# Kernel tuning notes

Measured on AMD Instinct MI355X. Metric: run time of the kernel, lower is better.

The kernel has to match this reference:

```python
import jax, jax.numpy as jnp
import numpy as np

WORD_DIM = 200
ASPECT_DIM = 32
NUM_NEG = 2
AVG_RATING = 3.8
LR_RATING = 1.0
LR_ABAE = 1.0


def setup_inputs() -> dict:
    key = jax.random.key(0)
    ks = jax.random.split(key, 20)
    R, L, D, A, B, NNZ = 20000, 30, WORD_DIM, ASPECT_DIM, 4096, 65536
    e_w = jax.random.normal(ks[0], (R, L, D), jnp.float32)
    y_s = jax.random.normal(ks[1], (R, D), jnp.float32)
    z_n = jax.random.normal(ks[2], (R * NUM_NEG, D), jnp.float32)
    label = jax.random.uniform(ks[3], (B,), jnp.float32, 1.0, 5.0)
    u_idx = jnp.stack([jax.random.randint(ks[4], (NNZ,), 0, B),
                       jax.random.randint(ks[5], (NNZ,), 0, R)]).astype(jnp.int64)
    i_idx = jnp.stack([jax.random.randint(ks[6], (NNZ,), 0, B),
                       jax.random.randint(ks[7], (NNZ,), 0, R)]).astype(jnp.int64)
    u_val = jax.random.uniform(ks[8], (NNZ,), jnp.float32)
    i_val = jax.random.uniform(ks[9], (NNZ,), jnp.float32)
    s = 0.05
    M_w = jax.random.normal(ks[10], (D, D), jnp.float32) * s
    M_b = jnp.zeros((D,), jnp.float32)
    W_w = jax.random.normal(ks[11], (A, D), jnp.float32) * s
    W_b = jnp.zeros((A,), jnp.float32)
    T_w = jax.random.normal(ks[12], (D, A), jnp.float32) * s
    T_b = jnp.zeros((D,), jnp.float32)
    fc_w = jax.random.uniform(ks[13], (1, A), jnp.float32, -0.05, 0.05)
    fc_b = jnp.zeros((1,), jnp.float32)
    fm_V = jax.random.uniform(ks[14], (A, 10), jnp.float32, -0.05, 0.05)
    return dict(e_w=e_w, y_s=y_s, z_n=z_n, label=label,
                user_histor_value=u_val, item_histor_value=i_val,
                M_w=M_w, M_b=M_b, W_w=W_w, W_b=W_b, T_w=T_w, T_b=T_b,
                fc_w=fc_w, fc_b=fc_b, fm_V=fm_V,
                user_histor_index=u_idx, item_histor_index=i_idx)


def _l2norm(x, axis):
    return x / jnp.maximum(jnp.linalg.norm(x, axis=axis, keepdims=True), 1e-12)


def reference(e_w, y_s, z_n, label, user_histor_value, item_histor_value,
              M_w, M_b, W_w, W_b, T_w, T_b, fc_w, fc_b, fm_V,
              user_histor_index, item_histor_index):
    R, L, D = e_w.shape
    A = W_w.shape[0]
    B = label.shape[0]
    # ABAE attention: dx = (e_w @ M^T + b) . y_s  -> (R, L)
    Me = jnp.einsum('rld,ed->rle', e_w, M_w) + M_b  # (R, L, D)
    dx = jnp.einsum('rld,rd->rl', Me, y_s)
    ax = jax.nn.softmax(dx, axis=1)                 # attention over words
    z_s = jnp.einsum('rld,rl->rd', e_w, ax)         # (R, D) weighted sentence emb
    p_t = z_s @ W_w.T + W_b                         # (R, A) aspect weights
    r_s = p_t @ T_w.T + T_b                         # (R, D) reconstructed emb
    # margin ranking (hinge) loss on cosine similarities
    c1 = jnp.sum(_l2norm(r_s, 1) * _l2norm(z_s, 1), axis=-1, keepdims=True)  # (R,1)
    c1 = jnp.tile(c1, (1, NUM_NEG)).reshape(-1)                              # (R*neg,)
    zn = _l2norm(z_n.reshape(R, NUM_NEG, D), 2)
    c2 = jnp.sum(zn * _l2norm(r_s, 1)[:, None, :], axis=-1).reshape(-1)
    abae_out_loss = jnp.maximum(0.0, 1.0 - (c1 - c2))
    J_loss = jnp.mean(abae_out_loss)
    # orthogonality regularizer on aspect matrix columns
    Tn = _l2norm(T_w, 0)                            # normalize each column (dim=0)
    G = Tn.T @ Tn                                   # (A, A)
    U_loss = jnp.mean((G - jnp.eye(A, dtype=G.dtype)) ** 2)
    abae_loss = U_loss + J_loss
    # sparse pooling: (B, R) sparse @ (R, A)
    u_rows, u_cols = user_histor_index[0], user_histor_index[1]
    i_rows, i_cols = item_histor_index[0], item_histor_index[1]
    user_aspect = jax.ops.segment_sum(p_t[u_cols] * user_histor_value[:, None],
                                      u_rows, num_segments=B)
    item_aspect = jax.ops.segment_sum(p_t[i_cols] * item_histor_value[:, None],
                                      i_rows, num_segments=B)
    output_emb = user_aspect * item_aspect          # (B, A)
    # factorization machine
    fm_linear = output_emb @ fc_w.T + fc_b          # (B, 1)
    i1 = (output_emb @ fm_V) ** 2
    i2 = (output_emb ** 2) @ (fm_V ** 2)
    # NOTE: faithful to source -- the 0.5*sum reduces over ALL elements (scalar)
    fm_output = 0.5 * jnp.sum(i1 - i2) + fm_linear  # (B, 1)
    prediction = fm_output + jnp.float32(AVG_RATING)
    rating_out_loss = (prediction.reshape(-1) - label) ** 2
    rating_loss = jnp.mean(rating_out_loss)
    obj = LR_RATING * rating_loss + LR_ABAE * abae_loss
    return (obj, rating_out_loss, abae_out_loss, prediction, user_aspect, item_aspect)
```

## Files before the change

### kernel.cpp

```cpp
#include <hip/hip_runtime.h>
#include <hip/hip_bf16.h>
#include <math.h>

#define R_CNT   20000
#define L_CNT   30
#define D_CNT   200
#define A_CNT   32
#define B_CNT   4096
#define NNZ_CNT 65536
#define AVG_RATING 3.8f

#define KA_GRID 768

#define OUT_OBJ  0
#define OUT_RL   1
#define OUT_AB   (1 + B_CNT)
#define OUT_PRED (OUT_AB + 2*R_CNT)
#define OUT_UA   (OUT_PRED + B_CNT)
#define OUT_IA   (OUT_UA + B_CNT*A_CNT)

#define WS_DBL    0
#define WS_MODE   32
#define WS_FMLIN  64
#define WS_PT     16448
#define WS_V      2576448
#define WS_JPART  18627648
#define WS_SPART  18667648
#define WS_UPART  18671744

#define BAR_LDS() do { asm volatile("s_waitcnt lgkmcnt(0)" ::: "memory"); \
                       __builtin_amdgcn_s_barrier(); \
                       __builtin_amdgcn_sched_barrier(0); } while (0)
#define BAR_TAIL() do { asm volatile("s_waitcnt vmcnt(1)" ::: "memory"); \
                        __builtin_amdgcn_s_barrier(); \
                        __builtin_amdgcn_sched_barrier(0); } while (0)

__device__ __forceinline__ float4 blk_reduce4(float4 v, float4* scratch) {
    __syncthreads();
    #pragma unroll
    for (int o = 32; o >= 1; o >>= 1) {
        v.x += __shfl_xor(v.x, o);
        v.y += __shfl_xor(v.y, o);
        v.z += __shfl_xor(v.z, o);
        v.w += __shfl_xor(v.w, o);
    }
    int w = threadIdx.x >> 6;
    if ((threadIdx.x & 63) == 0) scratch[w] = v;
    __syncthreads();
    float4 t0 = scratch[0], t1 = scratch[1], t2 = scratch[2], t3 = scratch[3];
    return make_float4(t0.x + t1.x + t2.x + t3.x,
                       t0.y + t1.y + t2.y + t3.y,
                       t0.z + t1.z + t2.z + t3.z,
                       t0.w + t1.w + t2.w + t3.w);
}

__global__ __launch_bounds__(256) void k_init(float* __restrict__ out,
                                              double* __restrict__ dbl,
                                              int* __restrict__ mode,
                                              const int* __restrict__ u_idx) {
    int gid = blockIdx.x * 256 + threadIdx.x;
    if (gid < 2 * B_CNT * A_CNT) out[OUT_UA + gid] = 0.f;
    if (gid == 0) {
        dbl[0] = 0.0; dbl[1] = 0.0; dbl[2] = 0.0;
        int m = 1;
        for (int i = 1; i < 256; i += 2) if (u_idx[i] != 0) { m = 0; break; }
        *mode = m;
    }
}

__global__ __launch_bounds__(256) void k_uloss(const float* __restrict__ T_w,
                                               float* __restrict__ upart) {
    __shared__ __align__(16) float Tsh[D_CNT * 32];
    __shared__ float tn[32];
    __shared__ float4 red4[4];
    int tid = threadIdx.x;
    for (int idx = tid; idx < 1600; idx += 256)
        ((float4*)Tsh)[idx] = ((const float4*)T_w)[idx];
    __syncthreads();
    int a = tid >> 3, k = tid & 7;
    float p = 0.f;
    #pragma unroll
    for (int j = 0; j < 25; ++j) { float t = Tsh[(k + 8*j)*32 + a]; p = fmaf(t, t, p); }
    p += __shfl_xor(p, 1); p += __shfl_xor(p, 2); p += __shfl_xor(p, 4);
    if (k == 0) tn[a] = fmaxf(sqrtf(p), 1e-12f);
    __syncthreads();
    const int i = blockIdx.x;
    float s = 0.f;
    #pragma unroll
    for (int j = 0; j < 25; ++j)
        s = fmaf(Tsh[(k + 8*j)*32 + i], Tsh[(k + 8*j)*32 + a], s);
    s += __shfl_xor(s, 1); s += __shfl_xor(s, 2); s += __shfl_xor(s, 4);
    float part = 0.f;
    if (k == 0) {
        float g = s / (tn[i] * tn[a]);
        float diff = g - ((i == a) ? 1.f : 0.f);
        part = diff * diff;
    }
    float4 tot = blk_reduce4(make_float4(part, 0.f, 0.f, 0.f), red4);
    if (tid == 0) upart[i] = tot.x;
}

__global__ __launch_bounds__(256) void k_vgemm(const float* __restrict__ y_s,
                                               const float* __restrict__ M_w,
                                               float* __restrict__ V) {
    __shared__ __align__(16) float Msh[25 * 260];
    __shared__ __align__(16) float Ysh[25 * 68];
    int tid = threadIdx.x;
    int r0 = blockIdx.x * 64;
    int dg = tid & 31, rg = tid >> 5;
    float acc[8][8];
    #pragma unroll
    for (int i = 0; i < 8; i++)
        #pragma unroll
        for (int j = 0; j < 8; j++) acc[i][j] = 0.f;

    for (int e0 = 0; e0 < D_CNT; e0 += 25) {
        __syncthreads();
        for (int idx = tid; idx < 25 * 256; idx += 256) {
            int ee = idx >> 8, d = idx & 255;
            Msh[ee * 260 + d] = (d < D_CNT) ? M_w[(e0 + ee) * D_CNT + d] : 0.f;
        }
        for (int idx = tid; idx < 25 * 64; idx += 256) {
            int rr = idx / 25, ee = idx - rr * 25;
            int row = r0 + rr;
            Ysh[ee * 68 + rr] = (row < R_CNT) ? y_s[row * D_CNT + e0 + ee] : 0.f;
        }
        __syncthreads();
        for (int ee = 0; ee < 25; ee++) {
            const float4 ya = *(const float4*)&Ysh[ee * 68 + rg * 8];
            const float4 yb = *(const float4*)&Ysh[ee * 68 + rg * 8 + 4];
            const float4 ma = *(const float4*)&Msh[ee * 260 + dg * 8];
            const float4 mb = *(const float4*)&Msh[ee * 260 + dg * 8 + 4];
            float ys[8] = {ya.x, ya.y, ya.z, ya.w, yb.x, yb.y, yb.z, yb.w};
            float ms[8] = {ma.x, ma.y, ma.z, ma.w, mb.x, mb.y, mb.z, mb.w};
            #pragma unroll
            for (int i = 0; i < 8; i++)
                #pragma unroll
                for (int j = 0; j < 8; j++)
                    acc[i][j] = fmaf(ys[i], ms[j], acc[i][j]);
        }
    }
    if (dg < 25) {
        #pragma unroll
        for (int i = 0; i < 8; i++) {
            int row = r0 + rg * 8 + i;
            if (row < R_CNT) {
                *(float4*)&V[row * D_CNT + dg * 8]     = make_float4(acc[i][0], acc[i][1], acc[i][2], acc[i][3]);
                *(float4*)&V[row * D_CNT + dg * 8 + 4] = make_float4(acc[i][4], acc[i][5], acc[i][6], acc[i][7]);
            }
        }
    }
}

__device__ __forceinline__ void stage_review(const float* __restrict__ ew_src,
                                             const float* __restrict__ v_src,
                                             float* ldsE, float* ldsV,
                                             int w, int lane) {
    #pragma unroll
    for (int i = 0; i < 6; ++i) {
        int c = w * 6 + i;
        int f4 = c * 64 + lane;
        if (f4 > 1499) f4 = 1499;
        __builtin_amdgcn_global_load_lds(
            (const __attribute__((address_space(1))) unsigned int*)(ew_src + (size_t)f4 * 4),
            (__attribute__((address_space(3))) unsigned int*)(ldsE + c * 256),
            16, 0, 0);
    }
    __builtin_amdgcn_global_load_lds(
        (const __attribute__((address_space(1))) unsigned int*)(v_src + w * 64 + lane),
        (__attribute__((address_space(3))) unsigned int*)(ldsV + w * 64),
        4, 0, 0);
}

__global__ __launch_bounds__(256) void k_attn(const float* __restrict__ e_w,
                                              const float* __restrict__ V,
                                              const float* __restrict__ z_n,
                                              const float* __restrict__ W_w,
                                              const float* __restrict__ W_b,
                                              const float* __restrict__ T_w,
                                              const float* __restrict__ T_b,
                                              float* __restrict__ p_t,
                                              float* __restrict__ out,
                                              double* __restrict__ jpart) {
    __shared__ __align__(16) float bufE[2][6144];
    __shared__ __align__(16) float bufV[2][256];
    __shared__ __align__(16) float zsh[D_CNT];
    __shared__ float axs[32], pts[32];
    __shared__ float4 red[8];
    const int tid = threadIdx.x;
    const int w = tid >> 6, lane = tid & 63;
    const float wb = W_b[tid >> 3];
    const float tb = (tid < D_CNT) ? T_b[tid] : 0.f;
    double jloc = 0.0;

    int r = blockIdx.x;
    stage_review(e_w + (size_t)r * 6000, V + (size_t)r * D_CNT,
                 bufE[0], bufV[0], w, lane);
    __syncthreads();
    int cur = 0;

    for (;;) {
        const int rn = r + KA_GRID;
        const bool have_next = (rn < R_CNT);

        float zn0 = 0.f, zn1 = 0.f;
        if (tid < D_CNT) {
            zn0 = z_n[(size_t)(2 * r) * D_CNT + tid];
            zn1 = z_n[(size_t)(2 * r + 1) * D_CNT + tid];
        }
        if (have_next)
            stage_review(e_w + (size_t)rn * 6000, V + (size_t)rn * D_CNT,
                         bufE[cur ^ 1], bufV[cur ^ 1], w, lane);

        const float* ew = bufE[cur];
        const float* vsh = bufV[cur];

        if (tid < 240) {
            int l = tid >> 3, k = tid & 7;
            float p = 0.f;
            #pragma unroll
            for (int j = 0; j < 25; ++j)
                p = fmaf(ew[l * 200 + k + 8 * j], vsh[k + 8 * j], p);
            p += __shfl_xor(p, 1); p += __shfl_xor(p, 2); p += __shfl_xor(p, 4);
            if (k == 0) axs[l] = p;
        }
        BAR_LDS();

        if (tid < 64) {
            float v = (tid < L_CNT) ? axs[tid] : -3.0e38f;
            float m = v;
            #pragma unroll
            for (int o = 32; o >= 1; o >>= 1) m = fmaxf(m, __shfl_xor(m, o));
            float e = (tid < L_CNT) ? __expf(v - m) : 0.f;
            float s = e;
            #pragma unroll
            for (int o = 32; o >= 1; o >>= 1) s += __shfl_xor(s, o);
            if (tid < L_CNT) axs[tid] = e / s;
        }
        BAR_LDS();

        float zreg = 0.f;
        if (tid < D_CNT) {
            #pragma unroll
            for (int l = 0; l < L_CNT; ++l)
                zreg = fmaf(ew[l * 200 + tid], axs[l], zreg);
            zsh[tid] = zreg;
        }
        BAR_LDS();

        {
            int a = tid >> 3, k = tid & 7;
            float p = 0.f;
            #pragma unroll
            for (int j = 0; j < 25; ++j)
                p = fmaf(zsh[k + 8 * j], W_w[a * 200 + k + 8 * j], p);
            p += __shfl_xor(p, 1); p += __shfl_xor(p, 2); p += __shfl_xor(p, 4);
            if (k == 0) {
                float pt = p + wb;
                pts[a] = pt;
                p_t[(size_t)r * 32 + a] = pt;
            }
        }
        BAR_LDS();

        float rv = 0.f;
        if (tid < D_CNT) {
            rv = tb;
            const float4* tw = (const float4*)(T_w + tid * 32);
            #pragma unroll
            for (int q = 0; q < 8; ++q) {
                float4 t = tw[q];
                rv = fmaf(t.x, pts[4 * q + 0], rv);
                rv = fmaf(t.y, pts[4 * q + 1], rv);
                rv = fmaf(t.z, pts[4 * q + 2], rv);
                rv = fmaf(t.w, pts[4 * q + 3], rv);
            }
        }
        float4 Av = make_float4(rv * rv, rv * zreg, zreg * zreg, zn0 * zn0);
        float4 Bv = make_float4(zn0 * rv, zn1 * zn1, zn1 * rv, 0.f);
        #pragma unroll
        for (int o = 32; o >= 1; o >>= 1) {
            Av.x += __shfl_xor(Av.x, o); Av.y += __shfl_xor(Av.y, o);
            Av.z += __shfl_xor(Av.z, o); Av.w += __shfl_xor(Av.w, o);
            Bv.x += __shfl_xor(Bv.x, o); Bv.y += __shfl_xor(Bv.y, o);
            Bv.z += __shfl_xor(Bv.z, o);
        }
        if ((tid & 63) == 0) { red[2 * w] = Av; red[2 * w + 1] = Bv; }
        BAR_LDS();
        if (tid == 0) {
            float rr = 0.f, rz = 0.f, zz = 0.f, n00 = 0.f, n0r = 0.f, n11 = 0.f, n1r = 0.f;
            #pragma unroll
            for (int i = 0; i < 4; ++i) {
                float4 a = red[2 * i], b = red[2 * i + 1];
                rr += a.x; rz += a.y; zz += a.z; n00 += a.w;
                n0r += b.x; n11 += b.y; n1r += b.z;
            }
            float nr = fmaxf(sqrtf(rr), 1e-12f);
            float nz = fmaxf(sqrtf(zz), 1e-12f);
            float c1  = rz  / (nr * nz);
            float c20 = n0r / (fmaxf(sqrtf(n00), 1e-12f) * nr);
            float c21 = n1r / (fmaxf(sqrtf(n11), 1e-12f) * nr);
            float l0 = fmaxf(0.f, 1.f - (c1 - c20));
            float l1 = fmaxf(0.f, 1.f - (c1 - c21));
            out[OUT_AB + 2 * r]     = l0;
            out[OUT_AB + 2 * r + 1] = l1;
            jloc += (double)l0 + (double)l1;
        }
        if (!have_next) break;
        BAR_TAIL();
        cur ^= 1; r = rn;
    }
    if (tid == 0) jpart[blockIdx.x] = jloc;
}

__global__ __launch_bounds__(256) void k_scatter(const int* __restrict__ u_idx,
                                                 const int* __restrict__ i_idx,
                                                 const float* __restrict__ u_val,
                                                 const float* __restrict__ i_val,
                                                 const float* __restrict__ p_t,
                                                 const int* __restrict__ mode,
                                                 float* __restrict__ out) {
    long long gid = (long long)blockIdx.x * 256 + threadIdx.x;
    const long long HALF = (long long)NNZ_CNT * 32;
    int is_item = gid >= HALF;
    long long rem = gid - (is_item ? HALF : 0);
    int k = (int)(rem >> 5), a = (int)(rem & 31);
    const int* idx = is_item ? i_idx : u_idx;
    const float* val = is_item ? i_val : u_val;
    int m64 = *mode;
    int row, col;
    if (m64) { row = idx[2 * k]; col = idx[2 * (NNZ_CNT + k)]; }
    else     { row = idx[k];     col = idx[NNZ_CNT + k]; }
    float v = p_t[col * 32 + a] * val[k];
    float* base = out + (is_item ? OUT_IA : OUT_UA);
    atomicAdd(&base[row * 32 + a], v);
}

__global__ __launch_bounds__(256) void k_fm(const float* __restrict__ out,
                                            const float* __restrict__ fc_w,
                                            const float* __restrict__ fc_b,
                                            const float* __restrict__ fm_V,
                                            float* __restrict__ fm_lin,
                                            double* __restrict__ spart) {
    __shared__ float parts[8];
    int tid = threadIdx.x;
    int a = tid & 31;
    int b = blockIdx.x * 8 + (tid >> 5);
    float ua = out[OUT_UA + b * 32 + a];
    float ia = out[OUT_IA + b * 32 + a];
    float oe = ua * ia;
    float oe2 = oe * oe;
    float lin = oe * fc_w[a];
    #pragma unroll
    for (int o = 1; o < 32; o <<= 1) lin += __shfl_xor(lin, o);
    float part = 0.f;
    #pragma unroll
    for (int j = 0; j < 10; j++) {
        float v = fm_V[a * 10 + j];
        float s1 = oe * v;
        float s2 = oe2 * v * v;
        #pragma unroll
        for (int o = 1; o < 32; o <<= 1) { s1 += __shfl_xor(s1, o); s2 += __shfl_xor(s2, o); }
        part += s1 * s1 - s2;
    }
    if (a == 0) {
        fm_lin[b] = lin + fc_b[0];
        parts[tid >> 5] = part;
    }
    __syncthreads();
    if (tid == 0) {
        float s = 0.f;
        #pragma unroll
        for (int i = 0; i < 8; ++i) s += parts[i];
        spart[blockIdx.x] = 0.5 * (double)s;
    }
}

__global__ __launch_bounds__(256) void k_pred(const float* __restrict__ label,
                                              const float* __restrict__ fm_lin,
                                              const double* __restrict__ spart,
                                              float* __restrict__ out,
                                              double* __restrict__ r_sum) {
    __shared__ double sred[4];
    __shared__ float4 red4[4];
    __shared__ float Ssh;
    int tid = threadIdx.x;
    double sl = spart[tid] + spart[tid + 256];
    #pragma unroll
    for (int o = 32; o >= 1; o >>= 1) sl += __shfl_xor(sl, o);
    if ((tid & 63) == 0) sred[tid >> 6] = sl;
    __syncthreads();
    if (tid == 0) Ssh = (float)(sred[0] + sred[1] + sred[2] + sred[3]);
    __syncthreads();
    float S = Ssh;
    int b = blockIdx.x * 256 + tid;
    float pred = fm_lin[b] + S + AVG_RATING;
    float d = pred - label[b];
    float rl = d * d;
    out[OUT_PRED + b] = pred;
    out[OUT_RL + b] = rl;
    float4 t = blk_reduce4(make_float4(rl, 0.f, 0.f, 0.f), red4);
    if (tid == 0) atomicAdd(r_sum, (double)t.x);
}

__global__ __launch_bounds__(256) void k_final(const double* __restrict__ dbl,
                                               const double* __restrict__ jpart,
                                               const float* __restrict__ upart,
                                               float* __restrict__ out) {
    __shared__ double jred[4];
    __shared__ float ured[4];
    int tid = threadIdx.x;
    double j = 0.0;
    for (int i = tid; i < KA_GRID; i += 256) j += jpart[i];
    float u = (tid < 32) ? upart[tid] : 0.f;
    #pragma unroll
    for (int o = 32; o >= 1; o >>= 1) { j += __shfl_xor(j, o); u += __shfl_xor(u, o); }
    if ((tid & 63) == 0) { jred[tid >> 6] = j; ured[tid >> 6] = u; }
    __syncthreads();
    if (tid == 0) {
        double J = (jred[0] + jred[1] + jred[2] + jred[3]) / (2.0 * R_CNT);
        double U = (double)(ured[0] + ured[1] + ured[2] + ured[3]) / 1024.0;
        double RL = dbl[2] / (double)B_CNT;
        out[OUT_OBJ] = (float)(RL + U + J);
    }
}

extern "C" void kernel_launch(void* const* d_in, const int* in_sizes, int n_in,
                              void* d_out, int out_size, void* d_ws, size_t ws_size,
                              hipStream_t stream) {
    const float* e_w   = (const float*)d_in[0];
    const float* y_s   = (const float*)d_in[1];
    const float* z_n   = (const float*)d_in[2];
    const float* label = (const float*)d_in[3];
    const float* u_val = (const float*)d_in[4];
    const float* i_val = (const float*)d_in[5];
    const float* M_w   = (const float*)d_in[6];
    const float* W_w   = (const float*)d_in[8];
    const float* W_b   = (const float*)d_in[9];
    const float* T_w   = (const float*)d_in[10];
    const float* T_b   = (const float*)d_in[11];
    const float* fc_w  = (const float*)d_in[12];
    const float* fc_b  = (const float*)d_in[13];
    const float* fm_V  = (const float*)d_in[14];
    const int*   u_idx = (const int*)d_in[15];
    const int*   i_idx = (const int*)d_in[16];

    float* out = (float*)d_out;
    char* ws = (char*)d_ws;
    double* dbl   = (double*)(ws + WS_DBL);
    int* mode     = (int*)(ws + WS_MODE);
    float* fm_lin = (float*)(ws + WS_FMLIN);
    float* p_t    = (float*)(ws + WS_PT);
    float* V      = (float*)(ws + WS_V);
    double* jpart = (double*)(ws + WS_JPART);
    double* spart = (double*)(ws + WS_SPART);
    float* upart  = (float*)(ws + WS_UPART);

    k_init<<<1024, 256, 0, stream>>>(out, dbl, mode, u_idx);
    k_vgemm<<<(R_CNT + 63) / 64, 256, 0, stream>>>(y_s, M_w, V);
    k_uloss<<<32, 256, 0, stream>>>(T_w, upart);
    k_attn<<<KA_GRID, 256, 0, stream>>>(e_w, V, z_n, W_w, W_b, T_w, T_b,
                                        p_t, out, jpart);
    k_scatter<<<(2 * NNZ_CNT * 32) / 256, 256, 0, stream>>>(u_idx, i_idx, u_val, i_val,
                                                            p_t, mode, out);
    k_fm<<<B_CNT / 8, 256, 0, stream>>>(out, fc_w, fc_b, fm_V, fm_lin, spart);
    k_pred<<<B_CNT / 256, 256, 0, stream>>>(label, fm_lin, spart, out, &dbl[2]);
    k_final<<<1, 256, 0, stream>>>(dbl, jpart, upart, out);
}
```

Baseline: 329.9 us.

## Fuse prologue and epilogue kernels; single-buffer attention with doubled grid

Merges k_init, k_vgemm and k_uloss into one k_pre launch, and merges k_pred and k_final into a single-block k_predfinal, cutting launch count. k_attn drops its double-buffered LDS staging in favour of one buffer that is refilled mid-iteration after the last use of e_w. That shrinks LDS so more blocks fit per CU, with the grid doubled to 1536 and a launch-bounds occupancy hint. The trade is less prefetch overlap per block in exchange for more resident blocks hiding latency, plus a serial single-block reduction at the end.

```diff
diff --git a/kernel.cpp b/kernel.cpp
--- a/kernel.cpp
+++ b/kernel.cpp
@@ -10,7 +10,7 @@
 #define NNZ_CNT 65536
 #define AVG_RATING 3.8f
 
-#define KA_GRID 768
+#define KA_GRID 1536
 
 #define OUT_OBJ  0
 #define OUT_RL   1
@@ -31,7 +31,7 @@
 #define BAR_LDS() do { asm volatile("s_waitcnt lgkmcnt(0)" ::: "memory"); \
                        __builtin_amdgcn_s_barrier(); \
                        __builtin_amdgcn_sched_barrier(0); } while (0)
-#define BAR_TAIL() do { asm volatile("s_waitcnt vmcnt(1)" ::: "memory"); \
+#define BAR_FULL() do { asm volatile("s_waitcnt vmcnt(0) lgkmcnt(0)" ::: "memory"); \
                         __builtin_amdgcn_s_barrier(); \
                         __builtin_amdgcn_sched_barrier(0); } while (0)
 
@@ -54,108 +54,109 @@
                        t0.w + t1.w + t2.w + t3.w);
 }
 
-__global__ __launch_bounds__(256) void k_init(float* __restrict__ out,
-                                              double* __restrict__ dbl,
-                                              int* __restrict__ mode,
-                                              const int* __restrict__ u_idx) {
-    int gid = blockIdx.x * 256 + threadIdx.x;
-    if (gid < 2 * B_CNT * A_CNT) out[OUT_UA + gid] = 0.f;
-    if (gid == 0) {
-        dbl[0] = 0.0; dbl[1] = 0.0; dbl[2] = 0.0;
-        int m = 1;
-        for (int i = 1; i < 256; i += 2) if (u_idx[i] != 0) { m = 0; break; }
-        *mode = m;
-    }
-}
-
-__global__ __launch_bounds__(256) void k_uloss(const float* __restrict__ T_w,
-                                               float* __restrict__ upart) {
-    __shared__ __align__(16) float Tsh[D_CNT * 32];
-    __shared__ float tn[32];
-    __shared__ float4 red4[4];
-    int tid = threadIdx.x;
-    for (int idx = tid; idx < 1600; idx += 256)
-        ((float4*)Tsh)[idx] = ((const float4*)T_w)[idx];
-    __syncthreads();
-    int a = tid >> 3, k = tid & 7;
-    float p = 0.f;
-    #pragma unroll
-    for (int j = 0; j < 25; ++j) { float t = Tsh[(k + 8*j)*32 + a]; p = fmaf(t, t, p); }
-    p += __shfl_xor(p, 1); p += __shfl_xor(p, 2); p += __shfl_xor(p, 4);
-    if (k == 0) tn[a] = fmaxf(sqrtf(p), 1e-12f);
-    __syncthreads();
-    const int i = blockIdx.x;
-    float s = 0.f;
-    #pragma unroll
-    for (int j = 0; j < 25; ++j)
-        s = fmaf(Tsh[(k + 8*j)*32 + i], Tsh[(k + 8*j)*32 + a], s);
-    s += __shfl_xor(s, 1); s += __shfl_xor(s, 2); s += __shfl_xor(s, 4);
-    float part = 0.f;
-    if (k == 0) {
-        float g = s / (tn[i] * tn[a]);
-        float diff = g - ((i == a) ? 1.f : 0.f);
-        part = diff * diff;
-    }
-    float4 tot = blk_reduce4(make_float4(part, 0.f, 0.f, 0.f), red4);
-    if (tid == 0) upart[i] = tot.x;
-}
-
-__global__ __launch_bounds__(256) void k_vgemm(const float* __restrict__ y_s,
-                                               const float* __restrict__ M_w,
-                                               float* __restrict__ V) {
-    __shared__ __align__(16) float Msh[25 * 260];
-    __shared__ __align__(16) float Ysh[25 * 68];
-    int tid = threadIdx.x;
-    int r0 = blockIdx.x * 64;
-    int dg = tid & 31, rg = tid >> 5;
-    float acc[8][8];
-    #pragma unroll
-    for (int i = 0; i < 8; i++)
-        #pragma unroll
-        for (int j = 0; j < 8; j++) acc[i][j] = 0.f;
-
-    for (int e0 = 0; e0 < D_CNT; e0 += 25) {
+__global__ __launch_bounds__(256) void k_pre(const float* __restrict__ y_s,
+                                             const float* __restrict__ M_w,
+                                             const float* __restrict__ T_w,
+                                             const int* __restrict__ u_idx,
+                                             float* __restrict__ V,
+                                             float* __restrict__ upart,
+                                             float* __restrict__ out,
+                                             double* __restrict__ dbl,
+                                             int* __restrict__ mode) {
+    __shared__ __align__(16) float sh[8224];
+    const int tid = threadIdx.x;
+    const int bid = blockIdx.x;
+
+    if (bid < 313) {
+        float* Msh = sh;
+        float* Ysh = sh + 6500;
+        int r0 = bid * 64;
+        int dg = tid & 31, rg = tid >> 5;
+        float acc[8][8];
+        #pragma unroll
+        for (int i = 0; i < 8; i++)
+            #pragma unroll
+            for (int j = 0; j < 8; j++) acc[i][j] = 0.f;
+        for (int e0 = 0; e0 < D_CNT; e0 += 25) {
+            __syncthreads();
+            for (int idx = tid; idx < 25 * 256; idx += 256) {
+                int ee = idx >> 8, d = idx & 255;
+                Msh[ee * 260 + d] = (d < D_CNT) ? M_w[(e0 + ee) * D_CNT + d] : 0.f;
+            }
+            for (int idx = tid; idx < 25 * 64; idx += 256) {
+                int rr = idx / 25, ee = idx - rr * 25;
+                int row = r0 + rr;
+                Ysh[ee * 68 + rr] = (row < R_CNT) ? y_s[row * D_CNT + e0 + ee] : 0.f;
+            }
+            __syncthreads();
+            for (int ee = 0; ee < 25; ee++) {
+                const float4 ya = *(const float4*)&Ysh[ee * 68 + rg * 8];
+                const float4 yb = *(const float4*)&Ysh[ee * 68 + rg * 8 + 4];
+                const float4 ma = *(const float4*)&Msh[ee * 260 + dg * 8];
+                const float4 mb = *(const float4*)&Msh[ee * 260 + dg * 8 + 4];
+                float ys[8] = {ya.x, ya.y, ya.z, ya.w, yb.x, yb.y, yb.z, yb.w};
+                float ms[8] = {ma.x, ma.y, ma.z, ma.w, mb.x, mb.y, mb.z, mb.w};
+                #pragma unroll
+                for (int i = 0; i < 8; i++)
+                    #pragma unroll
+                    for (int j = 0; j < 8; j++)
+                        acc[i][j] = fmaf(ys[i], ms[j], acc[i][j]);
+            }
+        }
+        if (dg < 25) {
+            #pragma unroll
+            for (int i = 0; i < 8; i++) {
+                int row = r0 + rg * 8 + i;
+                if (row < R_CNT) {
+                    *(float4*)&V[row * D_CNT + dg * 8]     = make_float4(acc[i][0], acc[i][1], acc[i][2], acc[i][3]);
+                    *(float4*)&V[row * D_CNT + dg * 8 + 4] = make_float4(acc[i][4], acc[i][5], acc[i][6], acc[i][7]);
+                }
+            }
+        }
+    } else if (bid < 345) {
+        float* Tsh = sh;
+        float* tn  = sh + 6400;
+        float4* red4 = (float4*)(sh + 6448);
+        for (int idx = tid; idx < 1600; idx += 256)
+            ((float4*)Tsh)[idx] = ((const float4*)T_w)[idx];
         __syncthreads();
-        for (int idx = tid; idx < 25 * 256; idx += 256) {
-            int ee = idx >> 8, d = idx & 255;
-            Msh[ee * 260 + d] = (d < D_CNT) ? M_w[(e0 + ee) * D_CNT + d] : 0.f;
-        }
-        for (int idx = tid; idx < 25 * 64; idx += 256) {
-            int rr = idx / 25, ee = idx - rr * 25;
-            int row = r0 + rr;
-            Ysh[ee * 68 + rr] = (row < R_CNT) ? y_s[row * D_CNT + e0 + ee] : 0.f;
-        }
+        int a = tid >> 3, k = tid & 7;
+        float p = 0.f;
+        #pragma unroll
+        for (int j = 0; j < 25; ++j) { float t = Tsh[(k + 8*j)*32 + a]; p = fmaf(t, t, p); }
+        p += __shfl_xor(p, 1); p += __shfl_xor(p, 2); p += __shfl_xor(p, 4);
+        if (k == 0) tn[a] = fmaxf(sqrtf(p), 1e-12f);
         __syncthreads();
-        for (int ee = 0; ee < 25; ee++) {
-            const float4 ya = *(const float4*)&Ysh[ee * 68 + rg * 8];
-            const float4 yb = *(const float4*)&Ysh[ee * 68 + rg * 8 + 4];
-            const float4 ma = *(const float4*)&Msh[ee * 260 + dg * 8];
-            const float4 mb = *(const float4*)&Msh[ee * 260 + dg * 8 + 4];
-            float ys[8] = {ya.x, ya.y, ya.z, ya.w, yb.x, yb.y, yb.z, yb.w};
-            float ms[8] = {ma.x, ma.y, ma.z, ma.w, mb.x, mb.y, mb.z, mb.w};
-            #pragma unroll
-            for (int i = 0; i < 8; i++)
-                #pragma unroll
-                for (int j = 0; j < 8; j++)
-                    acc[i][j] = fmaf(ys[i], ms[j], acc[i][j]);
-        }
-    }
-    if (dg < 25) {
-        #pragma unroll
-        for (int i = 0; i < 8; i++) {
-            int row = r0 + rg * 8 + i;
-            if (row < R_CNT) {
-                *(float4*)&V[row * D_CNT + dg * 8]     = make_float4(acc[i][0], acc[i][1], acc[i][2], acc[i][3]);
-                *(float4*)&V[row * D_CNT + dg * 8 + 4] = make_float4(acc[i][4], acc[i][5], acc[i][6], acc[i][7]);
-            }
-        }
-    }
-}
-
-__device__ __forceinline__ void stage_review(const float* __restrict__ ew_src,
-                                             const float* __restrict__ v_src,
-                                             float* ldsE, float* ldsV,
-                                             int w, int lane) {
+        const int i = bid - 313;
+        float s = 0.f;
+        #pragma unroll
+        for (int j = 0; j < 25; ++j)
+            s = fmaf(Tsh[(k + 8*j)*32 + i], Tsh[(k + 8*j)*32 + a], s);
+        s += __shfl_xor(s, 1); s += __shfl_xor(s, 2); s += __shfl_xor(s, 4);
+        float part = 0.f;
+        if (k == 0) {
+            float g = s / (tn[i] * tn[a]);
+            float diff = g - ((i == a) ? 1.f : 0.f);
+            part = diff * diff;
+        }
+        float4 tot = blk_reduce4(make_float4(part, 0.f, 0.f, 0.f), red4);
+        if (tid == 0) upart[i] = tot.x;
+    } else {
+        int base = (bid - 345) * 2048;
+        #pragma unroll
+        for (int j = 0; j < 8; ++j)
+            out[OUT_UA + base + j * 256 + tid] = 0.f;
+        if (bid == 345 && tid == 0) {
+            dbl[0] = 0.0; dbl[1] = 0.0; dbl[2] = 0.0;
+            int m = 1;
+            for (int i = 1; i < 256; i += 2) if (u_idx[i] != 0) { m = 0; break; }
+            *mode = m;
+        }
+    }
+}
+
+__device__ __forceinline__ void stage_E(const float* __restrict__ ew_src,
+                                        float* ldsE, int w, int lane) {
     #pragma unroll
     for (int i = 0; i < 6; ++i) {
         int c = w * 6 + i;
@@ -166,24 +167,27 @@
             (__attribute__((address_space(3))) unsigned int*)(ldsE + c * 256),
             16, 0, 0);
     }
+}
+__device__ __forceinline__ void stage_V(const float* __restrict__ v_src,
+                                        float* ldsV, int w, int lane) {
     __builtin_amdgcn_global_load_lds(
         (const __attribute__((address_space(1))) unsigned int*)(v_src + w * 64 + lane),
         (__attribute__((address_space(3))) unsigned int*)(ldsV + w * 64),
         4, 0, 0);
 }
 
-__global__ __launch_bounds__(256) void k_attn(const float* __restrict__ e_w,
-                                              const float* __restrict__ V,
-                                              const float* __restrict__ z_n,
-                                              const float* __restrict__ W_w,
-                                              const float* __restrict__ W_b,
-                                              const float* __restrict__ T_w,
-                                              const float* __restrict__ T_b,
-                                              float* __restrict__ p_t,
-                                              float* __restrict__ out,
-                                              double* __restrict__ jpart) {
-    __shared__ __align__(16) float bufE[2][6144];
-    __shared__ __align__(16) float bufV[2][256];
+__global__ __launch_bounds__(256, 6) void k_attn(const float* __restrict__ e_w,
+                                                 const float* __restrict__ V,
+                                                 const float* __restrict__ z_n,
+                                                 const float* __restrict__ W_w,
+                                                 const float* __restrict__ W_b,
+                                                 const float* __restrict__ T_w,
+                                                 const float* __restrict__ T_b,
+                                                 float* __restrict__ p_t,
+                                                 float* __restrict__ out,
+                                                 double* __restrict__ jpart) {
+    __shared__ __align__(16) float bufE[6144];
+    __shared__ __align__(16) float bufV[256];
     __shared__ __align__(16) float zsh[D_CNT];
     __shared__ float axs[32], pts[32];
     __shared__ float4 red[8];
@@ -194,10 +198,9 @@
     double jloc = 0.0;
 
     int r = blockIdx.x;
-    stage_review(e_w + (size_t)r * 6000, V + (size_t)r * D_CNT,
-                 bufE[0], bufV[0], w, lane);
-    __syncthreads();
-    int cur = 0;
+    stage_E(e_w + (size_t)r * 6000, bufE, w, lane);
+    stage_V(V + (size_t)r * D_CNT, bufV, w, lane);
+    __syncthreads();
 
     for (;;) {
         const int rn = r + KA_GRID;
@@ -208,19 +211,13 @@
             zn0 = z_n[(size_t)(2 * r) * D_CNT + tid];
             zn1 = z_n[(size_t)(2 * r + 1) * D_CNT + tid];
         }
-        if (have_next)
-            stage_review(e_w + (size_t)rn * 6000, V + (size_t)rn * D_CNT,
-                         bufE[cur ^ 1], bufV[cur ^ 1], w, lane);
-
-        const float* ew = bufE[cur];
-        const float* vsh = bufV[cur];
 
         if (tid < 240) {
             int l = tid >> 3, k = tid & 7;
             float p = 0.f;
             #pragma unroll
             for (int j = 0; j < 25; ++j)
-                p = fmaf(ew[l * 200 + k + 8 * j], vsh[k + 8 * j], p);
+                p = fmaf(bufE[l * 200 + k + 8 * j], bufV[k + 8 * j], p);
             p += __shfl_xor(p, 1); p += __shfl_xor(p, 2); p += __shfl_xor(p, 4);
             if (k == 0) axs[l] = p;
         }
@@ -243,10 +240,15 @@
         if (tid < D_CNT) {
             #pragma unroll
             for (int l = 0; l < L_CNT; ++l)
-                zreg = fmaf(ew[l * 200 + tid], axs[l], zreg);
+                zreg = fmaf(bufE[l * 200 + tid], axs[l], zreg);
             zsh[tid] = zreg;
         }
         BAR_LDS();
+
+        if (have_next) {
+            stage_E(e_w + (size_t)rn * 6000, bufE, w, lane);
+            stage_V(V + (size_t)rn * D_CNT, bufV, w, lane);
+        }
 
         {
             int a = tid >> 3, k = tid & 7;
@@ -286,7 +288,9 @@
             Bv.z += __shfl_xor(Bv.z, o);
         }
         if ((tid & 63) == 0) { red[2 * w] = Av; red[2 * w + 1] = Bv; }
-        BAR_LDS();
+
+        BAR_FULL();
+
         if (tid == 0) {
             float rr = 0.f, rz = 0.f, zz = 0.f, n00 = 0.f, n0r = 0.f, n11 = 0.f, n1r = 0.f;
             #pragma unroll
@@ -307,8 +311,7 @@
             jloc += (double)l0 + (double)l1;
         }
         if (!have_next) break;
-        BAR_TAIL();
-        cur ^= 1; r = rn;
+        r = rn;
     }
     if (tid == 0) jpart[blockIdx.x] = jloc;
 }
@@ -376,51 +379,58 @@
     }
 }
 
-__global__ __launch_bounds__(256) void k_pred(const float* __restrict__ label,
-                                              const float* __restrict__ fm_lin,
-                                              const double* __restrict__ spart,
-                                              float* __restrict__ out,
-                                              double* __restrict__ r_sum) {
-    __shared__ double sred[4];
-    __shared__ float4 red4[4];
+__global__ __launch_bounds__(256) void k_predfinal(const float* __restrict__ label,
+                                                   const float* __restrict__ fm_lin,
+                                                   const double* __restrict__ spart,
+                                                   const double* __restrict__ jpart,
+                                                   const float* __restrict__ upart,
+                                                   float* __restrict__ out) {
+    __shared__ double dred[4];
     __shared__ float Ssh;
     int tid = threadIdx.x;
     double sl = spart[tid] + spart[tid + 256];
     #pragma unroll
     for (int o = 32; o >= 1; o >>= 1) sl += __shfl_xor(sl, o);
-    if ((tid & 63) == 0) sred[tid >> 6] = sl;
-    __syncthreads();
-    if (tid == 0) Ssh = (float)(sred[0] + sred[1] + sred[2] + sred[3]);
+    if ((tid & 63) == 0) dred[tid >> 6] = sl;
+    __syncthreads();
+    if (tid == 0) Ssh = (float)(dred[0] + dred[1] + dred[2] + dred[3]);
     __syncthreads();
     float S = Ssh;
-    int b = blockIdx.x * 256 + tid;
-    float pred = fm_lin[b] + S + AVG_RATING;
-    float d = pred - label[b];
-    float rl = d * d;
-    out[OUT_PRED + b] = pred;
-    out[OUT_RL + b] = rl;
-    float4 t = blk_reduce4(make_float4(rl, 0.f, 0.f, 0.f), red4);
-    if (tid == 0) atomicAdd(r_sum, (double)t.x);
-}
-
-__global__ __launch_bounds__(256) void k_final(const double* __restrict__ dbl,
-                                               const double* __restrict__ jpart,
-                                               const float* __restrict__ upart,
-                                               float* __restrict__ out) {
-    __shared__ double jred[4];
+    double racc = 0.0;
+    #pragma unroll
+    for (int i = 0; i < 16; ++i) {
+        int b = tid + 256 * i;
+        float pred = fm_lin[b] + S + AVG_RATING;
+        float d = pred - label[b];
+        float rl = d * d;
+        out[OUT_PRED + b] = pred;
+        out[OUT_RL + b] = rl;
+        racc += (double)rl;
+    }
+    double jacc = 0.0;
+    for (int i = tid; i < KA_GRID; i += 256) jacc += jpart[i];
+    float u = (tid < 32) ? upart[tid] : 0.f;
+    #pragma unroll
+    for (int o = 32; o >= 1; o >>= 1) {
+        racc += __shfl_xor(racc, o);
+        jacc += __shfl_xor(jacc, o);
+        u    += __shfl_xor(u, o);
+    }
+    __syncthreads();
+    if ((tid & 63) == 0) dred[tid >> 6] = racc;
+    __syncthreads();
+    double rsum = dred[0] + dred[1] + dred[2] + dred[3];
+    __syncthreads();
+    if ((tid & 63) == 0) dred[tid >> 6] = jacc;
+    __syncthreads();
+    double jsum = dred[0] + dred[1] + dred[2] + dred[3];
     __shared__ float ured[4];
-    int tid = threadIdx.x;
-    double j = 0.0;
-    for (int i = tid; i < KA_GRID; i += 256) j += jpart[i];
-    float u = (tid < 32) ? upart[tid] : 0.f;
-    #pragma unroll
-    for (int o = 32; o >= 1; o >>= 1) { j += __shfl_xor(j, o); u += __shfl_xor(u, o); }
-    if ((tid & 63) == 0) { jred[tid >> 6] = j; ured[tid >> 6] = u; }
+    if ((tid & 63) == 0) ured[tid >> 6] = u;
     __syncthreads();
     if (tid == 0) {
-        double J = (jred[0] + jred[1] + jred[2] + jred[3]) / (2.0 * R_CNT);
         double U = (double)(ured[0] + ured[1] + ured[2] + ured[3]) / 1024.0;
-        double RL = dbl[2] / (double)B_CNT;
+        double J = jsum / (2.0 * R_CNT);
+        double RL = rsum / (double)B_CNT;
         out[OUT_OBJ] = (float)(RL + U + J);
     }
 }
@@ -456,14 +466,11 @@
     double* spart = (double*)(ws + WS_SPART);
     float* upart  = (float*)(ws + WS_UPART);
 
-    k_init<<<1024, 256, 0, stream>>>(out, dbl, mode, u_idx);
-    k_vgemm<<<(R_CNT + 63) / 64, 256, 0, stream>>>(y_s, M_w, V);
-    k_uloss<<<32, 256, 0, stream>>>(T_w, upart);
+    k_pre<<<473, 256, 0, stream>>>(y_s, M_w, T_w, u_idx, V, upart, out, dbl, mode);
     k_attn<<<KA_GRID, 256, 0, stream>>>(e_w, V, z_n, W_w, W_b, T_w, T_b,
                                         p_t, out, jpart);
     k_scatter<<<(2 * NNZ_CNT * 32) / 256, 256, 0, stream>>>(u_idx, i_idx, u_val, i_val,
                                                             p_t, mode, out);
     k_fm<<<B_CNT / 8, 256, 0, stream>>>(out, fc_w, fc_b, fm_V, fm_lin, spart);
-    k_pred<<<B_CNT / 256, 256, 0, stream>>>(label, fm_lin, spart, out, &dbl[2]);
-    k_final<<<1, 256, 0, stream>>>(dbl, jpart, upart, out);
-}
+    k_predfinal<<<1, 256, 0, stream>>>(label, fm_lin, spart, jpart, upart, out);
+}
```

New measurement: 370.2 us. 1.12x slower.
